# Kernel optimization log

Hardware: AMD Instinct MI355X
Metric: run time of the kernel (lower is better)

The kernel has to match this reference:

```python
import jax, jax.numpy as jnp
import numpy as np

BITS = (2, 4, 8)
GROUP = 4
EPS = 1e-5


def _ste_round(x):
    return x + jax.lax.stop_gradient(jnp.round(x) - x)


def _quant_act(x, b):
    s = float(2 ** b - 1)
    return _ste_round(jnp.clip(x, 0.0, 1.0) * s) / s


def _quant_weight(w, mean, std, b):
    # normalize by (mean, std) of the gating-selected channels, then b-bit uniform quant on [-1, 1]
    wn = jnp.clip((w - mean) / (std + EPS), -1.0, 1.0)
    s = float(2 ** b - 1)
    u = _ste_round((wn + 1.0) * 0.5 * s) / s
    return 2.0 * u - 1.0


def _mixed_qconv(x, w, w_mean, w_std, w_logits, a_logits):
    # bitwidth-selectable conv: softmax mixture over quantized weights / activations
    pw = jax.nn.softmax(w_logits)
    pa = jax.nn.softmax(a_logits)
    w_mix = sum(pw[i] * _quant_weight(w, w_mean, w_std, b) for i, b in enumerate(BITS))
    x_mix = sum(pa[i] * _quant_act(x, b) for i, b in enumerate(BITS))
    return jax.lax.conv_general_dilated(
        x_mix, w_mix, window_strides=(1, 1), padding='SAME',
        dimension_numbers=('NCHW', 'OIHW', 'NCHW'))


def _bn(x, g, b, m, v):
    inv = jax.lax.rsqrt(v + EPS)
    return (x - m[None, :, None, None]) * (g * inv)[None, :, None, None] + b[None, :, None, None]


def _masked_mean_std(w, mask):
    # mean/std over gate-selected filter slices; torch uses .data -> stop_gradient, unbiased std
    m = jnp.broadcast_to(mask, w.shape)
    cnt = jnp.sum(m)
    mean = jnp.sum(w * m) / cnt
    var = jnp.sum(m * (w - mean) ** 2) / (cnt - 1.0)
    return jax.lax.stop_gradient(mean), jax.lax.stop_gradient(jnp.sqrt(var))


def _indicator(w1, thr):
    n, c, h, wk = w1.shape
    fw = w1.reshape(n // GROUP, GROUP * c * h * wk)
    nf = fw / jnp.max(jnp.abs(fw))
    norm = jnp.sum(jnp.abs(nf), axis=1) / (GROUP * c * h * wk)  # [n_choices]
    soft = jax.nn.sigmoid(norm - thr)
    hard = (norm > thr).astype(w1.dtype)
    return hard - jax.lax.stop_gradient(soft) + soft  # STE indicator


def setup_inputs() -> dict:
    key = jax.random.key(0)
    ks = jax.random.split(key, 10)
    B, C, H, W = 64, 256, 32, 32
    return {
        'x': jax.random.normal(ks[0], (B, C, H, W), jnp.float32),
        'w1': jax.random.normal(ks[1], (C, C, 3, 3), jnp.float32) * 0.05,
        'w2': jax.random.normal(ks[2], (C, C, 3, 3), jnp.float32) * 0.05,
        'bn1_gamma': jnp.ones((C,), jnp.float32),
        'bn1_beta': jnp.zeros((C,), jnp.float32),
        'bn1_mean': jax.random.normal(ks[3], (C,), jnp.float32) * 0.1,
        'bn1_var': jax.random.uniform(ks[4], (C,), jnp.float32, 0.5, 1.5),
        'bn2_gamma': jnp.ones((C,), jnp.float32),
        'bn2_beta': jnp.zeros((C,), jnp.float32),
        'bn2_mean': jax.random.normal(ks[5], (C,), jnp.float32) * 0.1,
        'bn2_var': jax.random.uniform(ks[6], (C,), jnp.float32, 0.5, 1.5),
        'threshold': jnp.zeros((1,), jnp.float32),
        'w_logits1': jax.random.normal(ks[7], (3,), jnp.float32) * 0.1,
        'a_logits1': jax.random.normal(ks[8], (3,), jnp.float32) * 0.1,
        'w_logits2': jax.random.normal(ks[9], (3,), jnp.float32) * 0.1,
        'a_logits2': jnp.zeros((3,), jnp.float32),
    }


def reference(x, w1, w2, bn1_gamma, bn1_beta, bn1_mean, bn1_var,
              bn2_gamma, bn2_beta, bn2_mean, bn2_var, threshold,
              w_logits1, a_logits1, w_logits2, a_logits2):
    thr = threshold[0]
    ind = _indicator(w1, thr)                       # [n_choices]
    ind_ch = jnp.repeat(ind, GROUP)                 # [out_plane]
    gate_mask = jax.lax.stop_gradient((ind_ch > 0).astype(x.dtype))

    # both_preact path
    residual = x
    h = jax.nn.relu(_bn(x, bn1_gamma, bn1_beta, bn1_mean, bn1_var))
    m1, s1 = _masked_mean_std(w1, gate_mask[:, None, None, None])
    h = _mixed_qconv(h, w1, m1, s1, w_logits1, a_logits1)
    h = jax.nn.relu(_bn(h, bn2_gamma, bn2_beta, bn2_mean, bn2_var))
    m2, s2 = _masked_mean_std(w2, gate_mask[None, :, None, None])
    h = h * ind_ch[None, :, None, None]             # differentiable channel gating
    h = _mixed_qconv(h, w2, m2, s2, w_logits2, a_logits2)
    return h + residual
```

## Files before the change

### kernel.cpp

```cpp
#include <hip/hip_runtime.h>
#include <stdint.h>

#define EPSF 1e-5f

typedef _Float16 h8_t __attribute__((ext_vector_type(8)));
typedef float f4_t __attribute__((ext_vector_type(4)));

#define BB 64
#define CC 256
#define HH 32
#define WW 32
#define HP 34
#define WP 34
#define PADIMG (HP*WP*CC)
#define PADTOT (BB*PADIMG)

#define S_GSUM   0
#define S_GMAX   64
#define S_W1S    128
#define S_W1Q    192
#define S_W2S    256
#define S_W2Q    320
#define S_PA2    384
#define S_INDCH  400
#define S_BN2SC  656
#define S_BN2SH  912

#define OFF_STATS 0
#define OFF_A1    8192
#define OFF_A2    (OFF_A1 + PADTOT*2)
#define OFF_W1T   (OFF_A2 + PADTOT*2)
#define OFF_W2T   (OFF_W1T + 9*CC*CC*2)

__device__ __forceinline__ void async_load16(void* lds, const void* g) {
  __builtin_amdgcn_global_load_lds(
      reinterpret_cast<uint32_t __attribute__((address_space(1)))*>((uintptr_t)g),
      reinterpret_cast<uint32_t __attribute__((address_space(3)))*>((uint32_t)(uintptr_t)lds),
      16, 0, 0);
}

#define WAITV4() asm volatile("s_waitcnt vmcnt(4)" ::: "memory")
#define WAITV0() asm volatile("s_waitcnt vmcnt(0)" ::: "memory")

__device__ __forceinline__ float wave_sum(float v) {
  for (int o = 32; o; o >>= 1) v += __shfl_down(v, o);
  return v;
}
__device__ __forceinline__ float wave_max(float v) {
  for (int o = 32; o; o >>= 1) v = fmaxf(v, __shfl_down(v, o));
  return v;
}

__device__ __forceinline__ void softmax3(const float* l, float* out) {
  float m = fmaxf(fmaxf(l[0], l[1]), l[2]);
  float e0 = expf(l[0] - m), e1 = expf(l[1] - m), e2 = expf(l[2] - m);
  float inv = 1.f / (e0 + e1 + e2);
  out[0] = e0 * inv; out[1] = e1 * inv; out[2] = e2 * inv;
}

__device__ __forceinline__ float qmix_act(float v, float p0, float p1, float p2) {
  float cl = fminf(fmaxf(v, 0.f), 1.f);
  return p0 * (rintf(cl * 3.f) / 3.f) + p1 * (rintf(cl * 15.f) / 15.f)
       + p2 * (rintf(cl * 255.f) / 255.f);
}

__global__ void k_stats(const float* __restrict__ w1, const float* __restrict__ w2,
                        float* stats) {
  __shared__ float red[4][4];
  int bid = blockIdx.x, t = threadIdx.x;
  int lane = t & 63, w = t >> 6;
  if (bid < 64) {
    const float* p = w1 + bid * 9216;
    float sa = 0.f, s = 0.f, q = 0.f, mx = 0.f;
    for (int i = t; i < 9216; i += 256) {
      float v = p[i];
      float a = fabsf(v);
      sa += a; s += v; q += v * v; mx = fmaxf(mx, a);
    }
    sa = wave_sum(sa); s = wave_sum(s); q = wave_sum(q); mx = wave_max(mx);
    if (lane == 0) { red[w][0] = sa; red[w][1] = s; red[w][2] = q; red[w][3] = mx; }
    __syncthreads();
    if (t == 0) {
      float a = 0, b = 0, c = 0, d = 0;
      for (int k = 0; k < 4; ++k) {
        a += red[k][0]; b += red[k][1]; c += red[k][2]; d = fmaxf(d, red[k][3]);
      }
      stats[S_GSUM + bid] = a;
      stats[S_W1S + bid] = b;
      stats[S_W1Q + bid] = c;
      stats[S_GMAX + bid] = d;
    }
  } else {
    int g = bid - 64;
    const float* p = w2 + (size_t)t * 2304 + g * 36;
    float s = 0.f, q = 0.f;
#pragma unroll
    for (int i = 0; i < 36; ++i) { float v = p[i]; s += v; q += v * v; }
    s = wave_sum(s); q = wave_sum(q);
    if (lane == 0) { red[w][0] = s; red[w][1] = q; }
    __syncthreads();
    if (t == 0) {
      float a = 0, b = 0;
      for (int k = 0; k < 4; ++k) { a += red[k][0]; b += red[k][1]; }
      stats[S_W2S + g] = a;
      stats[S_W2Q + g] = b;
    }
  }
}

#define WPS 264
#define APR_STRIDE 264
__global__ void k_fused(const float* __restrict__ w1, const float* __restrict__ w2,
                        const float* __restrict__ xin, const float* __restrict__ thr_p,
                        const float* __restrict__ bn1g, const float* __restrict__ bn1b,
                        const float* __restrict__ bn1m, const float* __restrict__ bn1v,
                        const float* __restrict__ bn2g, const float* __restrict__ bn2b,
                        const float* __restrict__ bn2m, const float* __restrict__ bn2v,
                        const float* __restrict__ wl1, const float* __restrict__ al1,
                        const float* __restrict__ wl2, const float* __restrict__ al2,
                        float* __restrict__ stats,
                        _Float16* __restrict__ wt1, _Float16* __restrict__ wt2,
                        _Float16* __restrict__ a1, _Float16* __restrict__ a2) {
  int bid = blockIdx.x, t = threadIdx.x;

  if (bid == 0) {
    __shared__ float sind[64];
    if (t < 64) {
      float thr = thr_p[0];
      float mx = wave_max(stats[S_GMAX + t]);
      mx = __shfl(mx, 0);
      float norm = stats[S_GSUM + t] / mx / 9216.0f;
      float soft = 1.f / (1.f + expf(-(norm - thr)));
      float hard = (norm > thr) ? 1.f : 0.f;
      sind[t] = (hard - soft) + soft;
    }
    __syncthreads();
    stats[S_INDCH + t] = sind[t >> 2];
    float sc2 = bn2g[t] * (1.f / sqrtf(bn2v[t] + EPSF));
    stats[S_BN2SC + t] = sc2;
    stats[S_BN2SH + t] = bn2b[t] - bn2m[t] * sc2;
    if (t == 0) softmax3(al2, stats + S_PA2);
    return;
  }

  if (bid <= 512) {
    __shared__ __attribute__((aligned(16))) _Float16 lds[9 * WPS];
    __shared__ float sM, sSD, sP[3];
    int which = (bid - 1) >> 8, o = (bid - 1) & 255;
    if (t < 64) {
      float thr = thr_p[0];
      float mx = wave_max(stats[S_GMAX + t]);
      mx = __shfl(mx, 0);
      float norm = stats[S_GSUM + t] / mx / 9216.0f;
      float soft = 1.f / (1.f + expf(-(norm - thr)));
      float hard = (norm > thr) ? 1.f : 0.f;
      float iv = (hard - soft) + soft;
      float gate = (iv > 0.f) ? 1.f : 0.f;
      float ng = wave_sum(gate);
      float s = wave_sum(gate * stats[(which ? S_W2S : S_W1S) + t]);
      float q = wave_sum(gate * stats[(which ? S_W2Q : S_W1Q) + t]);
      if (t == 0) {
        float cnt = ng * 9216.0f;
        float m = s / cnt;
        float v = (q - cnt * m * m) / (cnt - 1.0f);
        sM = m; sSD = sqrtf(fmaxf(v, 0.f));
        softmax3(which ? wl2 : wl1, sP);
      }
    }
    __syncthreads();
    const float* w = (which ? w2 : w1) + (size_t)o * 2304;
    float mean = sM, sd = sSD + EPSF;
    float p0 = sP[0], p1 = sP[1], p2 = sP[2];
#pragma unroll
    for (int it = 0; it < 9; ++it) {
      int f = it * 256 + t;
      float v = w[f];
      float wn = fminf(fmaxf((v - mean) / sd, -1.f), 1.f);
      float u0 = rintf((wn + 1.f) * 0.5f * 3.f) / 3.f;
      float u1 = rintf((wn + 1.f) * 0.5f * 15.f) / 15.f;
      float u2 = rintf((wn + 1.f) * 0.5f * 255.f) / 255.f;
      float mix = p0 * (2.f * u0 - 1.f) + p1 * (2.f * u1 - 1.f) + p2 * (2.f * u2 - 1.f);
      int ci = f / 9;
      int e = f - 9 * ci;
      lds[e * WPS + ci] = (_Float16)mix;
    }
    __syncthreads();
    _Float16* dst0 = (which ? wt2 : wt1) + o * 256;
#pragma unroll
    for (int it = 0; it < 2; ++it) {
      int qid = it * 256 + t;
      if (qid < 288) {
        int e = qid >> 5, c8 = (qid & 31) * 8;
        *(h8_t*)(dst0 + e * 65536 + c8) = *(const h8_t*)(lds + e * WPS + c8);
      }
    }
    return;
  }

  int ab = bid - 513;
  if (ab >= BB * HH) {
    int b = ab - BB * HH;
    _Float16* img = (b >= BB ? a2 : a1) + (size_t)(b & 63) * PADIMG;
    uint64_t* u = (uint64_t*)img;
#pragma unroll
    for (int it = 0; it < 17; ++it) {
      int idx = it * 256 + t;
      int r33 = (idx >= 2176);
      u[(size_t)(r33 ? 33 * WP * 64 : 0) + (idx - (r33 ? 2176 : 0))] = 0ull;
    }
#pragma unroll
    for (int it = 0; it < 16; ++it) {
      int idx = it * 256 + t;
      int p = idx >> 6;
      int y = 1 + (p >> 1), x = (p & 1) ? 33 : 0;
      u[(size_t)(y * WP + x) * 64 + (idx & 63)] = 0ull;
    }
    return;
  }

  __shared__ __attribute__((aligned(16))) _Float16 lds[32 * APR_STRIDE];
  __shared__ float sBsc[256], sBsh[256], sPa[3];
  {
    float sc1 = bn1g[t] * (1.f / sqrtf(bn1v[t] + EPSF));
    sBsc[t] = sc1;
    sBsh[t] = bn1b[t] - bn1m[t] * sc1;
    if (t == 0) softmax3(al1, sPa);
  }
  __syncthreads();
  int n = ab >> 5, y = ab & 31;
  int x4 = (t & 7) * 4, c0 = t >> 3;
  float pa0 = sPa[0], pa1 = sPa[1], pa2 = sPa[2];
#pragma unroll
  for (int it = 0; it < 8; ++it) {
    int c = it * 32 + c0;
    const float* src = xin + ((size_t)(n * CC + c) * HH + y) * WW + x4;
    float4 v = *(const float4*)src;
    float sc = sBsc[c], sh = sBsh[c];
#pragma unroll
    for (int k = 0; k < 4; ++k) {
      float q = qmix_act((&v.x)[k] * sc + sh, pa0, pa1, pa2);
      lds[(x4 + k) * APR_STRIDE + c] = (_Float16)q;
    }
  }
  __syncthreads();
  _Float16* orow = a1 + ((size_t)(n * HP + (y + 1)) * WP + 1) * CC;
#pragma unroll
  for (int it = 0; it < 4; ++it) {
    int qid = it * 256 + t;
    int xx = qid >> 5, c8 = (qid & 31) * 8;
    *(h8_t*)(orow + xx * CC + c8) = *(const h8_t*)(lds + xx * APR_STRIDE + c8);
  }
}

template <bool SW>
__global__ __launch_bounds__(256) void k_conv(
    const _Float16* __restrict__ act,
    const _Float16* __restrict__ wts,
    const float* __restrict__ stats,
    _Float16* __restrict__ a2out,
    const float* __restrict__ resid,
    float* __restrict__ out) {
  __shared__ __attribute__((aligned(16))) _Float16 AT[204 * 64];
  __shared__ __attribute__((aligned(16))) _Float16 WB[2 * 128 * 64];
  const int tid = threadIdx.x;
  const int lane = tid & 63, wid = tid >> 6;
  const int xcd = blockIdx.x & 7;
  const int j = blockIdx.x >> 3;
  const int blk_co = j >> 6;
  const int blk_m = xcd * 64 + (j & 63);

  const int srow = wid * 8 + (lane >> 3);
  const int g = (lane & 7) ^ (lane >> 3);
  int wbase[4];
#pragma unroll
  for (int q = 0; q < 4; ++q)
    wbase[q] = (blk_co * 128 + q * 32 + srow) * CC + g * 8;

  const int n0 = blk_m >> 3;
  const int y0 = (blk_m & 7) * 4;
  const _Float16* actbase = act + (size_t)(n0 * HP + y0) * WP * CC;

  const int wr = wid >> 1, wc = wid & 1;
  const int mrow = (SW ? wc : wr) * 64;
  const int wrow = (SW ? wr : wc) * 64;
  const int ksl = lane >> 4;

  int trbase[4], woff[4];
#pragma unroll
  for (int i = 0; i < 4; ++i) {
    int r = mrow + i * 16 + (lane & 15);
    trbase[i] = (r >> 5) * 34 + (r & 31);
    int rb = wrow + i * 16 + (lane & 15);
    woff[i] = rb * 64 + ((ksl ^ (lane & 7)) * 8);
  }

  f4_t acc[4][4];
  const f4_t z4 = {0.f, 0.f, 0.f, 0.f};
#pragma unroll
  for (int i = 0; i < 4; ++i)
#pragma unroll
    for (int j2 = 0; j2 < 4; ++j2) acc[i][j2] = z4;

  auto stageW = [&](int kcn, int en, int nb_) {
    const int wo = en * (CC * CC) + kcn * 64;
    _Float16* dst = WB + nb_ * (128 * 64);
#pragma unroll
    for (int q = 0; q < 4; ++q)
      async_load16(dst + (q * 32 + wid * 8) * 64, wts + wbase[q] + wo);
  };
  auto stageA = [&](int kcn) {
    const int kb = kcn * 64;
#pragma unroll
    for (int it = 0; it < 6; ++it) {
      int l = it * 256 + tid;
      int tr = l >> 3, gg = l & 7;
      int yl = tr / 34, px = tr - yl * 34;
      async_load16(AT + l * 8,
                   actbase + ((size_t)yl * WP + px) * CC + kb + ((gg ^ (tr & 7)) * 8));
    }
    if (tid < 96) {
      int l = 1536 + tid;
      int tr = l >> 3, gg = l & 7;
      int yl = tr / 34, px = tr - yl * 34;
      async_load16(AT + l * 8,
                   actbase + ((size_t)yl * WP + px) * CC + kb + ((gg ^ (tr & 7)) * 8));
    }
  };

  stageA(0);
  stageW(0, 0, 0);
  int nb = 0;
#pragma unroll 1
  for (int kc = 0; kc < 4; ++kc) {
#pragma unroll
    for (int e = 0; e < 9; ++e) {
      if (e < 8) {
        stageW(kc, e + 1, nb ^ 1);
        WAITV4();
      } else if (kc < 3) {
        stageW(kc + 1, 0, nb ^ 1);
        WAITV4();
      } else {
        WAITV0();
      }
      __builtin_amdgcn_s_barrier();
      asm volatile("" ::: "memory");
      __builtin_amdgcn_sched_barrier(0);

      const int de = (e / 3) * 34 + (e % 3);
      const _Float16* WBc = WB + nb * (128 * 64);
      __builtin_amdgcn_s_setprio(1);
      int aoff[4];
#pragma unroll
      for (int i = 0; i < 4; ++i) {
        int tr = trbase[i] + de;
        aoff[i] = tr * 64 + ((ksl ^ (tr & 7)) * 8);
      }
#pragma unroll
      for (int kk = 0; kk < 2; ++kk) {
        h8_t fa[4], fw[4];
#pragma unroll
        for (int i = 0; i < 4; ++i) {
          fa[i] = *(const h8_t*)(AT + (aoff[i] ^ (kk * 32)));
          fw[i] = *(const h8_t*)(WBc + (woff[i] ^ (kk * 32)));
        }
#pragma unroll
        for (int i = 0; i < 4; ++i)
#pragma unroll
          for (int j2 = 0; j2 < 4; ++j2)
            acc[i][j2] = __builtin_amdgcn_mfma_f32_16x16x32_f16(
                SW ? fw[i] : fa[i], SW ? fa[j2] : fw[j2], acc[i][j2], 0, 0, 0);
      }
      __builtin_amdgcn_s_setprio(0);
      asm volatile("" ::: "memory");
      __builtin_amdgcn_s_barrier();
      __builtin_amdgcn_sched_barrier(0);
      nb ^= 1;
    }
    if (kc < 3) stageA(kc + 1);
  }

  const int quad = lane >> 4;
  const int cq = lane & 15;
  if (!SW) {
    const float pa0 = stats[S_PA2], pa1 = stats[S_PA2 + 1], pa2 = stats[S_PA2 + 2];
#pragma unroll
    for (int j2 = 0; j2 < 4; ++j2) {
      const int co = blk_co * 128 + wc * 64 + j2 * 16 + cq;
      const float sc = stats[S_BN2SC + co];
      const float sh = stats[S_BN2SH + co];
      const float ic = stats[S_INDCH + co];
#pragma unroll
      for (int i = 0; i < 4; ++i) {
        const int mbase = blk_m * 128 + wr * 64 + i * 16 + quad * 4;
#pragma unroll
        for (int rg = 0; rg < 4; ++rg) {
          const int m = mbase + rg;
          const int n = m >> 10, y = (m >> 5) & 31, x = m & 31;
          float h = fmaxf(acc[i][j2][rg] * sc + sh, 0.f) * ic;
          float q = qmix_act(h, pa0, pa1, pa2);
          a2out[((size_t)(n * HP + y + 1) * WP + (x + 1)) * CC + co] = (_Float16)q;
        }
      }
    }
  } else {
#pragma unroll
    for (int j2 = 0; j2 < 4; ++j2) {
      const int m = blk_m * 128 + wc * 64 + j2 * 16 + cq;
      const int n = m >> 10, y = (m >> 5) & 31, x = m & 31;
#pragma unroll
      for (int i = 0; i < 4; ++i) {
        const int cobase = blk_co * 128 + wr * 64 + i * 16 + quad * 4;
#pragma unroll
        for (int rg = 0; rg < 4; ++rg) {
          const int co = cobase + rg;
          const int idx = ((n * CC + co) << 10) + (y << 5) + x;
          out[idx] = acc[i][j2][rg] + resid[idx];
        }
      }
    }
  }
}

extern "C" void kernel_launch(void* const* d_in, const int* in_sizes, int n_in,
                              void* d_out, int out_size, void* d_ws, size_t ws_size,
                              hipStream_t stream) {
  const float* x    = (const float*)d_in[0];
  const float* w1   = (const float*)d_in[1];
  const float* w2   = (const float*)d_in[2];
  const float* bn1g = (const float*)d_in[3];
  const float* bn1b = (const float*)d_in[4];
  const float* bn1m = (const float*)d_in[5];
  const float* bn1v = (const float*)d_in[6];
  const float* bn2g = (const float*)d_in[7];
  const float* bn2b = (const float*)d_in[8];
  const float* bn2m = (const float*)d_in[9];
  const float* bn2v = (const float*)d_in[10];
  const float* thr  = (const float*)d_in[11];
  const float* wl1  = (const float*)d_in[12];
  const float* al1  = (const float*)d_in[13];
  const float* wl2  = (const float*)d_in[14];
  const float* al2  = (const float*)d_in[15];

  char* ws = (char*)d_ws;
  float* stats = (float*)(ws + OFF_STATS);
  _Float16* a1 = (_Float16*)(ws + OFF_A1);
  _Float16* a2 = (_Float16*)(ws + OFF_A2);
  _Float16* wt1 = (_Float16*)(ws + OFF_W1T);
  _Float16* wt2 = (_Float16*)(ws + OFF_W2T);
  float* out = (float*)d_out;

  k_stats<<<128, 256, 0, stream>>>(w1, w2, stats);
  k_fused<<<1 + 512 + BB * HH + 128, 256, 0, stream>>>(
      w1, w2, x, thr, bn1g, bn1b, bn1m, bn1v, bn2g, bn2b, bn2m, bn2v,
      wl1, al1, wl2, al2, stats, wt1, wt2, a1, a2);
  k_conv<false><<<1024, 256, 0, stream>>>(a1, wt1, stats, a2, nullptr, nullptr);
  k_conv<true><<<1024, 256, 0, stream>>>(a2, wt2, stats, nullptr, x, out);
}
```

Before: 362.1 us.

## Load conv weights directly into registers in MFMA-fragment layout, drop weight LDS staging

The weight-prep kernel now writes quantized weights in a layout that matches the MFMA fragment order, so each lane can read its weight fragments straight from global memory into registers. The conv kernel drops the double-buffered weight LDS tile and its per-tap barriers, prefetching the next tap's weight fragments while the current tap's MFMAs run. Only one barrier pair per 64-channel chunk remains, around the activation restage, and the activation tile's staging loop is padded to a uniform seven iterations. This removes LDS write/read traffic and most barriers. In exchange it adds register pressure and relies on L2 and global-load latency being hidden by the software prefetch.

```diff
diff --git a/kernel.cpp b/kernel.cpp
--- a/kernel.cpp
+++ b/kernel.cpp
@@ -39,8 +39,7 @@
       16, 0, 0);
 }
 
-#define WAITV4() asm volatile("s_waitcnt vmcnt(4)" ::: "memory")
-#define WAITV0() asm volatile("s_waitcnt vmcnt(0)" ::: "memory")
+#define WAITV(N) asm volatile("s_waitcnt vmcnt(" #N ")" ::: "memory")
 
 __device__ __forceinline__ float wave_sum(float v) {
   for (int o = 32; o; o >>= 1) v += __shfl_down(v, o);
@@ -185,13 +184,14 @@
       lds[e * WPS + ci] = (_Float16)mix;
     }
     __syncthreads();
-    _Float16* dst0 = (which ? wt2 : wt1) + o * 256;
+    _Float16* dstW = (which ? wt2 : wt1);
 #pragma unroll
     for (int it = 0; it < 2; ++it) {
       int qid = it * 256 + t;
       if (qid < 288) {
-        int e = qid >> 5, c8 = (qid & 31) * 8;
-        *(h8_t*)(dst0 + e * 65536 + c8) = *(const h8_t*)(lds + e * WPS + c8);
+        int e = qid >> 5, cq = qid & 31;
+        *(h8_t*)(dstW + ((size_t)(e * 32 + cq) * 256 + o) * 8) =
+            *(const h8_t*)(lds + e * WPS + cq * 8);
       }
     }
     return;
@@ -260,8 +260,7 @@
     _Float16* __restrict__ a2out,
     const float* __restrict__ resid,
     float* __restrict__ out) {
-  __shared__ __attribute__((aligned(16))) _Float16 AT[204 * 64];
-  __shared__ __attribute__((aligned(16))) _Float16 WB[2 * 128 * 64];
+  __shared__ __attribute__((aligned(16))) _Float16 AT[224 * 64];
   const int tid = threadIdx.x;
   const int lane = tid & 63, wid = tid >> 6;
   const int xcd = blockIdx.x & 7;
@@ -269,13 +268,6 @@
   const int blk_co = j >> 6;
   const int blk_m = xcd * 64 + (j & 63);
 
-  const int srow = wid * 8 + (lane >> 3);
-  const int g = (lane & 7) ^ (lane >> 3);
-  int wbase[4];
-#pragma unroll
-  for (int q = 0; q < 4; ++q)
-    wbase[q] = (blk_co * 128 + q * 32 + srow) * CC + g * 8;
-
   const int n0 = blk_m >> 3;
   const int y0 = (blk_m & 7) * 4;
   const _Float16* actbase = act + (size_t)(n0 * HP + y0) * WP * CC;
@@ -285,14 +277,13 @@
   const int wrow = (SW ? wr : wc) * 64;
   const int ksl = lane >> 4;
 
-  int trbase[4], woff[4];
+  int trbase[4];
 #pragma unroll
   for (int i = 0; i < 4; ++i) {
     int r = mrow + i * 16 + (lane & 15);
     trbase[i] = (r >> 5) * 34 + (r & 31);
-    int rb = wrow + i * 16 + (lane & 15);
-    woff[i] = rb * 64 + ((ksl ^ (lane & 7)) * 8);
-  }
+  }
+  const unsigned vbase = (unsigned)(ksl * 256 + blk_co * 128 + wrow + (lane & 15)) * 8u;
 
   f4_t acc[4][4];
   const f4_t z4 = {0.f, 0.f, 0.f, 0.f};
@@ -301,83 +292,87 @@
 #pragma unroll
     for (int j2 = 0; j2 < 4; ++j2) acc[i][j2] = z4;
 
-  auto stageW = [&](int kcn, int en, int nb_) {
-    const int wo = en * (CC * CC) + kcn * 64;
-    _Float16* dst = WB + nb_ * (128 * 64);
-#pragma unroll
-    for (int q = 0; q < 4; ++q)
-      async_load16(dst + (q * 32 + wid * 8) * 64, wts + wbase[q] + wo);
-  };
   auto stageA = [&](int kcn) {
     const int kb = kcn * 64;
 #pragma unroll
-    for (int it = 0; it < 6; ++it) {
+    for (int it = 0; it < 7; ++it) {
       int l = it * 256 + tid;
       int tr = l >> 3, gg = l & 7;
       int yl = tr / 34, px = tr - yl * 34;
       async_load16(AT + l * 8,
                    actbase + ((size_t)yl * WP + px) * CC + kb + ((gg ^ (tr & 7)) * 8));
     }
-    if (tid < 96) {
-      int l = 1536 + tid;
-      int tr = l >> 3, gg = l & 7;
-      int yl = tr / 34, px = tr - yl * 34;
-      async_load16(AT + l * 8,
-                   actbase + ((size_t)yl * WP + px) * CC + kb + ((gg ^ (tr & 7)) * 8));
-    }
   };
 
+  h8_t fwA[4], fwB[4];
+  auto loadW = [&](h8_t* dst, int e, int kcn, int kk) {
+    const _Float16* p = wts + (size_t)((e * 32 + kcn * 8 + kk * 4) * 2048) + vbase;
+#pragma unroll
+    for (int i = 0; i < 4; ++i)
+      dst[i] = *(const h8_t*)(p + i * 128);
+  };
+
+  auto step = [&](const h8_t* fw, int e, int kk) {
+    const int de = (e / 3) * 34 + (e % 3);
+    h8_t fa[4];
+#pragma unroll
+    for (int i = 0; i < 4; ++i) {
+      int tr = trbase[i] + de;
+      fa[i] = *(const h8_t*)(AT + ((tr * 64 + ((ksl ^ (tr & 7)) * 8)) ^ (kk * 32)));
+    }
+    __builtin_amdgcn_s_setprio(1);
+#pragma unroll
+    for (int i = 0; i < 4; ++i)
+#pragma unroll
+      for (int j2 = 0; j2 < 4; ++j2)
+        acc[i][j2] = __builtin_amdgcn_mfma_f32_16x16x32_f16(
+            SW ? fw[i] : fa[i], SW ? fa[j2] : fw[j2], acc[i][j2], 0, 0, 0);
+    __builtin_amdgcn_s_setprio(0);
+  };
+
   stageA(0);
-  stageW(0, 0, 0);
-  int nb = 0;
+  loadW(fwA, 0, 0, 0);
+  loadW(fwB, 0, 0, 1);
+
 #pragma unroll 1
   for (int kc = 0; kc < 4; ++kc) {
-#pragma unroll
-    for (int e = 0; e < 9; ++e) {
-      if (e < 8) {
-        stageW(kc, e + 1, nb ^ 1);
-        WAITV4();
-      } else if (kc < 3) {
-        stageW(kc + 1, 0, nb ^ 1);
-        WAITV4();
+    WAITV(4);
+    __builtin_amdgcn_s_barrier();
+    __builtin_amdgcn_sched_barrier(0);
+#pragma unroll
+    for (int t2 = 0; t2 < 9; ++t2) {
+      if (t2 < 8) {
+        step(fwA, t2, 0);
+        loadW(fwA, t2 + 1, kc, 0);
+        step(fwB, t2, 1);
+        loadW(fwB, t2 + 1, kc, 1);
       } else {
-        WAITV0();
-      }
-      __builtin_amdgcn_s_barrier();
-      asm volatile("" ::: "memory");
-      __builtin_amdgcn_sched_barrier(0);
-
-      const int de = (e / 3) * 34 + (e % 3);
-      const _Float16* WBc = WB + nb * (128 * 64);
-      __builtin_amdgcn_s_setprio(1);
-      int aoff[4];
-#pragma unroll
-      for (int i = 0; i < 4; ++i) {
-        int tr = trbase[i] + de;
-        aoff[i] = tr * 64 + ((ksl ^ (tr & 7)) * 8);
-      }
-#pragma unroll
-      for (int kk = 0; kk < 2; ++kk) {
-        h8_t fa[4], fw[4];
+        step(fwA, 8, 0);
+        if (kc < 3) loadW(fwA, 0, kc + 1, 0);
+        h8_t faB[4];
 #pragma unroll
         for (int i = 0; i < 4; ++i) {
-          fa[i] = *(const h8_t*)(AT + (aoff[i] ^ (kk * 32)));
-          fw[i] = *(const h8_t*)(WBc + (woff[i] ^ (kk * 32)));
+          int tr = trbase[i] + 70;
+          faB[i] = *(const h8_t*)(AT + ((tr * 64 + ((ksl ^ (tr & 7)) * 8)) ^ 32));
         }
+        if (kc < 3) {
+          asm volatile("s_waitcnt lgkmcnt(0)" ::: "memory");
+          __builtin_amdgcn_sched_barrier(0);
+          __builtin_amdgcn_s_barrier();
+          __builtin_amdgcn_sched_barrier(0);
+          stageA(kc + 1);
+        }
+        __builtin_amdgcn_s_setprio(1);
 #pragma unroll
         for (int i = 0; i < 4; ++i)
 #pragma unroll
           for (int j2 = 0; j2 < 4; ++j2)
             acc[i][j2] = __builtin_amdgcn_mfma_f32_16x16x32_f16(
-                SW ? fw[i] : fa[i], SW ? fa[j2] : fw[j2], acc[i][j2], 0, 0, 0);
-      }
-      __builtin_amdgcn_s_setprio(0);
-      asm volatile("" ::: "memory");
-      __builtin_amdgcn_s_barrier();
-      __builtin_amdgcn_sched_barrier(0);
-      nb ^= 1;
-    }
-    if (kc < 3) stageA(kc + 1);
+                SW ? fwB[i] : faB[i], SW ? faB[j2] : fwB[j2], acc[i][j2], 0, 0, 0);
+        __builtin_amdgcn_s_setprio(0);
+        if (kc < 3) loadW(fwB, 0, kc + 1, 1);
+      }
+    }
   }
 
   const int quad = lane >> 4;
```

Result: slower. 371.3 us (+2.6%).
